# Optimization experiments

Measured on AMD Instinct MI355X. Metric: run time of the kernel, lower is better.

Reference implementation:

```python
import jax, jax.numpy as jnp
import numpy as np
from jax import lax

WINDOW = 40          # plan.window_size
E = 8                # len(plan.expand_feature)
F = 64               # len(plan.feature)
OUT_CH = 128
KERNEL = 5
ALPHA = 0.01         # leaky_relu_alpha
N_LABEL = 1


def time_conv(x, conv_size):
    """x: [N, T, F] -> [N, WINDOW, 5*E] sliding-window stats over first E features."""
    N, T, _ = x.shape
    begin = T - (conv_size + WINDOW - 1)
    xe = x[:, :, :E]                                             # [N, T, E]
    idx = begin + jnp.arange(WINDOW)[:, None] + jnp.arange(conv_size)[None, :]  # [W, C]
    win = xe[:, idx, :]                                          # [N, W, C, E]
    _mean = win.mean(axis=2)                                     # [N, W, E]
    _std = jnp.std(win, axis=2, ddof=1)                          # torch.std is unbiased
    _max = win.max(axis=2)
    _min = win.min(axis=2)
    # rank of last timestep of each window, cross-sectionally over stocks (dim 0)
    last = xe[:, begin + conv_size - 1: begin + conv_size - 1 + WINDOW, :]  # [N, W, E]
    order = jnp.argsort(-last, axis=0)
    rank = jnp.argsort(order, axis=0).astype(x.dtype) / N        # [N, W, E]
    return jnp.concatenate([_mean, _std, rank, _max, _min], axis=2)  # [N, W, 5E]


def setup_inputs() -> dict:
    key = jax.random.key(0)
    k1, k2, k3, k4, k5 = jax.random.split(key, 5)
    N, T = 8000, 64
    in_ch = F + 10 * E  # 144
    x = jax.random.normal(k1, (N, T, F), dtype=jnp.float32)
    conv_w = jax.random.normal(k2, (OUT_CH, in_ch, KERNEL), dtype=jnp.float32) * 0.05
    conv_b = jax.random.normal(k3, (OUT_CH,), dtype=jnp.float32) * 0.05
    lin_in = WINDOW + 1 - KERNEL  # 36
    lin_w = jax.random.normal(k4, (N_LABEL, lin_in), dtype=jnp.float32) * 0.1
    lin_b = jax.random.normal(k5, (N_LABEL,), dtype=jnp.float32) * 0.1
    return {"x": x, "conv_w": conv_w, "conv_b": conv_b, "lin_w": lin_w, "lin_b": lin_b}


def reference(x, conv_w, conv_b, lin_w, lin_b):
    week_x = time_conv(x, conv_size=5)     # [N, W, 5E]
    month_x = time_conv(x, conv_size=20)   # [N, W, 5E]
    xc = jnp.concatenate([x[:, -WINDOW:, :], week_x, month_x], axis=2)  # [N, W, F+10E]
    cnn_x = jnp.transpose(xc, (0, 2, 1))   # [N, C, W]
    part = lax.conv_general_dilated(cnn_x, conv_w, window_strides=(1,),
                                    padding='VALID',
                                    dimension_numbers=('NCH', 'OIH', 'NCH'))
    part = part + conv_b[None, :, None]    # [N, OUT_CH, W+1-K]
    h = part[:, -1, :]                     # last output channel, [N, W+1-K]
    h = jnp.where(h >= 0, h, ALPHA * h)    # leaky relu
    return h @ lin_w.T + lin_b             # [N, N_LABEL]
```

## Files before the change

### kernel.cpp

```cpp
#include <hip/hip_runtime.h>
#include <math.h>

#define NS    8000
#define TT    64
#define FF    64
#define EE    8
#define WIN   40
#define TR    59
#define NBINS 2048

#define XET_SZ  (8*59*8000)
#define RNK_SZ  (8*40*8000)

__global__ __launch_bounds__(256) void k_transpose(const float* __restrict__ x,
                                                   float* __restrict__ xeT) {
    int n = blockIdx.x * 256 + threadIdx.x;
    int r = blockIdx.y;
    if (n >= NS) return;
    const float* row = x + (size_t)n * (TT * FF) + (5 + r) * FF;
    float4 a = *(const float4*)(row);
    float4 b = *(const float4*)(row + 4);
    xeT[(0 * TR + r) * NS + n] = a.x;
    xeT[(1 * TR + r) * NS + n] = a.y;
    xeT[(2 * TR + r) * NS + n] = a.z;
    xeT[(3 * TR + r) * NS + n] = a.w;
    xeT[(4 * TR + r) * NS + n] = b.x;
    xeT[(5 * TR + r) * NS + n] = b.y;
    xeT[(6 * TR + r) * NS + n] = b.z;
    xeT[(7 * TR + r) * NS + n] = b.w;
}

__device__ __forceinline__ int binOf(float v) {
    int b = (int)((v + 4.0f) * 256.0f);
    b = b < 0 ? 0 : b;
    return b > (NBINS - 1) ? (NBINS - 1) : b;
}

__global__ __launch_bounds__(1024) void k_rank(const float* __restrict__ xeT,
                                               float* __restrict__ rankT) {
    const int w = blockIdx.x;
    const int e = blockIdx.y;
    __shared__ unsigned hist[NBINS];
    __shared__ unsigned basev[NBINS];
    __shared__ unsigned bendv[NBINS];
    __shared__ float          sk[NS];
    __shared__ unsigned short si[NS];
    __shared__ unsigned wsum[16];

    const int tid  = threadIdx.x;
    const int lane = tid & 63;
    const int wid  = tid >> 6;
    const float* col = xeT + ((size_t)e * TR + (19 + w)) * NS;

    float val[8];
#pragma unroll
    for (int i = 0; i < 8; i++) {
        int idx = tid + i * 1024;
        val[i] = (idx < NS) ? col[idx] : 0.0f;
    }
    hist[tid] = 0;
    hist[tid + 1024] = 0;
    __syncthreads();

#pragma unroll
    for (int i = 0; i < 8; i++) {
        int idx = tid + i * 1024;
        if (idx < NS) atomicAdd(&hist[binOf(val[i])], 1u);
    }
    __syncthreads();

    unsigned h0 = hist[2 * tid + 0];
    unsigned h1 = hist[2 * tid + 1];
    unsigned cs = h0 + h1;
    unsigned sc = cs;
#pragma unroll
    for (int d = 1; d < 64; d <<= 1) {
        unsigned t2 = __shfl_up(sc, d);
        if (lane >= d) sc += t2;
    }
    if (lane == 63) wsum[wid] = sc;
    __syncthreads();
    unsigned woff = 0;
    for (int i = 0; i < wid; i++) woff += wsum[i];
    unsigned before = woff + (sc - cs);
    {
        int b = 2 * tid;
        bendv[b] = NS - before; before += h0; basev[b] = NS - before;
        hist[b] = basev[b];  b++;
        bendv[b] = NS - before; before += h1; basev[b] = NS - before;
        hist[b] = basev[b];
    }
    __syncthreads();

#pragma unroll
    for (int i = 0; i < 8; i++) {
        int idx = tid + i * 1024;
        if (idx < NS) {
            int b = binOf(val[i]);
            unsigned p = atomicAdd(&hist[b], 1u);
            sk[p] = val[i];
            si[p] = (unsigned short)idx;
        }
    }
    __syncthreads();

    float* outp = rankT + ((size_t)e * WIN + w) * NS;
#pragma unroll 1
    for (int i = 0; i < 8; i++) {
        int p = tid + i * 1024;
        if (p < NS) {
            float v = sk[p];
            unsigned idm = si[p];
            int b = binOf(v);
            unsigned lo = basev[b], hi = bendv[b];
            unsigned c = 0;
            for (unsigned q = lo; q < hi; q++) {
                float u2 = sk[q];
                c += (u2 > v) || (u2 == v && si[q] < idm);
            }
            outp[idm] = (float)(basev[b] + c) / 8000.0f;
        }
    }
}

__global__ __launch_bounds__(256) void k_raw(const float* __restrict__ x,
                                             const float* __restrict__ cw,
                                             float* __restrict__ uraw) {
    const int n    = blockIdx.x * 4 + (threadIdx.x >> 6);
    const int lane = threadIdx.x & 63;
    const int g    = lane >> 4;
    const int l    = lane & 15;
    const float* W = cw + 127 * 144 * 5;

    float wreg[20];
    {
        const float4* Wq = (const float4*)(W + l * 20);
#pragma unroll
        for (int q = 0; q < 5; q++) {
            float4 t = Wq[q];
            wreg[q * 4 + 0] = t.x; wreg[q * 4 + 1] = t.y;
            wreg[q * 4 + 2] = t.z; wreg[q * 4 + 3] = t.w;
        }
    }

    const float* xbase = x + (size_t)n * (TT * FF) + 24 * FF + l * 4;
    float* ubase = uraw + (size_t)n * (WIN * 5);

#pragma unroll 1
    for (int w0 = 0; w0 < WIN; w0 += 4) {
        const int w = w0 + g;
        float4 xv = *(const float4*)(xbase + w * FF);
        float acc[5];
#pragma unroll
        for (int k = 0; k < 5; k++) {
            acc[k] = xv.x * wreg[0 * 5 + k] + xv.y * wreg[1 * 5 + k]
                   + xv.z * wreg[2 * 5 + k] + xv.w * wreg[3 * 5 + k];
        }
#pragma unroll
        for (int d = 1; d < 16; d <<= 1) {
#pragma unroll
            for (int k = 0; k < 5; k++) acc[k] += __shfl_xor(acc[k], d, 64);
        }
        if (l < 5) {
            float v = acc[0];
            if (l == 1) v = acc[1];
            else if (l == 2) v = acc[2];
            else if (l == 3) v = acc[3];
            else if (l == 4) v = acc[4];
            ubase[w * 5 + l] = v;
        }
    }
}

__global__ __launch_bounds__(256) void k_der_final(const float* __restrict__ cw,
                                                   const float* __restrict__ xeT,
                                                   const float* __restrict__ rankT,
                                                   const float* __restrict__ uraw,
                                                   const float* __restrict__ cb,
                                                   const float* __restrict__ lw,
                                                   const float* __restrict__ lb,
                                                   float* __restrict__ outp) {
    __shared__ float red[8][32][37];
    const int tid = threadIdx.x;
    const int e   = tid >> 5;
    const int nl  = tid & 31;
    const int n0  = blockIdx.x * 32;
    const int n   = n0 + nl;
    const float* W = cw + 127 * 144 * 5;

    float gder[36];
#pragma unroll
    for (int j = 0; j < 36; j++) gder[j] = 0.0f;

    const float* col = xeT + (size_t)e * TR * NS + n;
    const float* rkp = rankT + (size_t)e * WIN * NS + n;

    float ring[20];
#pragma unroll
    for (int r = 0; r < 19; r++) ring[r] = col[(size_t)r * NS];

#pragma unroll
    for (int w = 0; w < WIN; w++) {
        ring[(w + 19) % 20] = col[(size_t)(w + 19) * NS];
        float s20 = 0.f, mn20 = ring[0], mx20 = ring[0];
#pragma unroll
        for (int i = 0; i < 20; i++) {
            float v = ring[i];
            s20 += v; mn20 = fminf(mn20, v); mx20 = fmaxf(mx20, v);
        }
        float m20 = s20 * (1.0f / 20.0f);
        float d20 = 0.f;
#pragma unroll
        for (int i = 0; i < 20; i++) { float t = ring[i] - m20; d20 += t * t; }
        float sd20 = sqrtf(d20 * (1.0f / 19.0f));

        float s5 = 0.f, mn5 = ring[(w + 15) % 20], mx5 = mn5;
#pragma unroll
        for (int i = 15; i < 20; i++) {
            float v = ring[(w + i) % 20];
            s5 += v; mn5 = fminf(mn5, v); mx5 = fmaxf(mx5, v);
        }
        float m5 = s5 * 0.2f;
        float d5 = 0.f;
#pragma unroll
        for (int i = 15; i < 20; i++) {
            float t = ring[(w + i) % 20] - m5; d5 += t * t;
        }
        float sd5 = sqrtf(d5 * 0.25f);

        float rk = rkp[(size_t)w * NS];

#pragma unroll
        for (int k = 0; k < 5; k++) {
            int j = w - k;
            if (j >= 0 && j < 36) {
                float uk;
                uk  = m5   * W[(64  + e) * 5 + k];
                uk += sd5  * W[(72  + e) * 5 + k];
                uk += rk   * (W[(80 + e) * 5 + k] + W[(120 + e) * 5 + k]);
                uk += mx5  * W[(88  + e) * 5 + k];
                uk += mn5  * W[(96  + e) * 5 + k];
                uk += m20  * W[(104 + e) * 5 + k];
                uk += sd20 * W[(112 + e) * 5 + k];
                uk += mx20 * W[(128 + e) * 5 + k];
                uk += mn20 * W[(136 + e) * 5 + k];
                gder[j] += uk;
            }
        }
    }

#pragma unroll
    for (int j = 0; j < 36; j++) red[e][nl][j] = gder[j];
    __syncthreads();

    for (int p = tid; p < 32 * 36; p += 256) {
        int nl2 = p / 36, j = p - nl2 * 36;
        float sum = 0.f;
#pragma unroll
        for (int e2 = 0; e2 < 8; e2++) sum += red[e2][nl2][j];
        red[0][nl2][j] = sum;
    }
    __syncthreads();

    if (tid < 32) {
        const float* ur = uraw + (size_t)n * (WIN * 5);
        float b127 = cb[127];
        float acc = lb[0];
#pragma unroll
        for (int j = 0; j < 36; j++) {
            float g = b127 + red[0][tid][j];
#pragma unroll
            for (int k = 0; k < 5; k++) g += ur[(j + k) * 5 + k];
            g = (g >= 0.0f) ? g : 0.01f * g;
            acc += g * lw[j];
        }
        outp[n] = acc;
    }
}

extern "C" void kernel_launch(void* const* d_in, const int* in_sizes, int n_in,
                              void* d_out, int out_size, void* d_ws, size_t ws_size,
                              hipStream_t stream) {
    const float* x  = (const float*)d_in[0];
    const float* cw = (const float*)d_in[1];
    const float* cb = (const float*)d_in[2];
    const float* lw = (const float*)d_in[3];
    const float* lb = (const float*)d_in[4];
    float* outp = (float*)d_out;

    float* ws    = (float*)d_ws;
    float* xeT   = ws;
    float* rankT = ws + XET_SZ;
    float* uraw  = ws + XET_SZ + RNK_SZ;

    k_transpose<<<dim3(32, 59), 256, 0, stream>>>(x, xeT);
    k_rank<<<dim3(WIN, EE), 1024, 0, stream>>>(xeT, rankT);
    k_raw<<<2000, 256, 0, stream>>>(x, cw, uraw);
    k_der_final<<<250, 256, 0, stream>>>(cw, xeT, rankT, uraw, cb, lw, lb, outp);
}
```

Measured before the change: 253.0 us.

## Fuse raw conv projection into transpose, pack rank keys, widen histogram bins

Merges the raw-feature projection of the last conv channel into the transpose kernel, so the separate k_raw launch goes away and x rows already loaded are reused. The rank kernel now uses 8192 finer histogram bins and packs value and index into one 64-bit sortable key, so the tie-break inside a bucket becomes a single integer compare and the bucket ends come from neighbouring bases. The per-channel conv weights are hoisted into registers in the final kernel. Risks are the extra register pressure and uncoalesced per-thread row loads in the fused kernel, plus the larger shared-memory footprint of the 64-bit keys and bigger histogram.

Measured after the change: 244.7 us. 1.03x faster.

```diff
diff --git a/kernel.cpp b/kernel.cpp
--- a/kernel.cpp
+++ b/kernel.cpp
@@ -7,13 +7,15 @@
 #define EE    8
 #define WIN   40
 #define TR    59
-#define NBINS 2048
+#define NBINS 8192
 
 #define XET_SZ  (8*59*8000)
 #define RNK_SZ  (8*40*8000)
 
-__global__ __launch_bounds__(256) void k_transpose(const float* __restrict__ x,
-                                                   float* __restrict__ xeT) {
+__global__ __launch_bounds__(256) void k0(const float* __restrict__ x,
+                                          const float* __restrict__ cw,
+                                          float* __restrict__ xeT,
+                                          float* __restrict__ uraw) {
     int n = blockIdx.x * 256 + threadIdx.x;
     int r = blockIdx.y;
     if (n >= NS) return;
@@ -28,12 +30,40 @@
     xeT[(5 * TR + r) * NS + n] = b.y;
     xeT[(6 * TR + r) * NS + n] = b.z;
     xeT[(7 * TR + r) * NS + n] = b.w;
+
+    if (r >= 19) {
+        const int w = r - 19;
+        const float* W = cw + 127 * 144 * 5;
+        float4 v[16];
+        v[0] = a; v[1] = b;
+#pragma unroll
+        for (int q = 2; q < 16; q++) v[q] = *(const float4*)(row + 4 * q);
+        float acc0 = 0.f, acc1 = 0.f, acc2 = 0.f, acc3 = 0.f, acc4 = 0.f;
+#pragma unroll
+        for (int q = 0; q < 16; q++) {
+            const float* Wq = W + (4 * q) * 5;
+            acc0 += v[q].x * Wq[0]  + v[q].y * Wq[5]  + v[q].z * Wq[10] + v[q].w * Wq[15];
+            acc1 += v[q].x * Wq[1]  + v[q].y * Wq[6]  + v[q].z * Wq[11] + v[q].w * Wq[16];
+            acc2 += v[q].x * Wq[2]  + v[q].y * Wq[7]  + v[q].z * Wq[12] + v[q].w * Wq[17];
+            acc3 += v[q].x * Wq[3]  + v[q].y * Wq[8]  + v[q].z * Wq[13] + v[q].w * Wq[18];
+            acc4 += v[q].x * Wq[4]  + v[q].y * Wq[9]  + v[q].z * Wq[14] + v[q].w * Wq[19];
+        }
+        float* o = uraw + ((size_t)n * WIN + w) * 5;
+        o[0] = acc0; o[1] = acc1; o[2] = acc2; o[3] = acc3; o[4] = acc4;
+    }
 }
 
 __device__ __forceinline__ int binOf(float v) {
-    int b = (int)((v + 4.0f) * 256.0f);
+    int b = (int)((v + 4.0f) * 1024.0f);
     b = b < 0 ? 0 : b;
     return b > (NBINS - 1) ? (NBINS - 1) : b;
+}
+
+__device__ __forceinline__ unsigned long long keyOf(float v, unsigned idx) {
+    unsigned s = __float_as_uint(v);
+    unsigned m = (s & 0x80000000u) ? (~s) : (s | 0x80000000u);
+    unsigned md = ~m;
+    return ((unsigned long long)md << 13) | idx;
 }
 
 __global__ __launch_bounds__(1024) void k_rank(const float* __restrict__ xeT,
@@ -42,9 +72,7 @@
     const int e = blockIdx.y;
     __shared__ unsigned hist[NBINS];
     __shared__ unsigned basev[NBINS];
-    __shared__ unsigned bendv[NBINS];
-    __shared__ float          sk[NS];
-    __shared__ unsigned short si[NS];
+    __shared__ unsigned long long sk[NS];
     __shared__ unsigned wsum[16];
 
     const int tid  = threadIdx.x;
@@ -58,8 +86,8 @@
         int idx = tid + i * 1024;
         val[i] = (idx < NS) ? col[idx] : 0.0f;
     }
-    hist[tid] = 0;
-    hist[tid + 1024] = 0;
+#pragma unroll
+    for (int j = 0; j < 8; j++) hist[tid + j * 1024] = 0;
     __syncthreads();
 
 #pragma unroll
@@ -69,9 +97,12 @@
     }
     __syncthreads();
 
-    unsigned h0 = hist[2 * tid + 0];
-    unsigned h1 = hist[2 * tid + 1];
-    unsigned cs = h0 + h1;
+    unsigned h[8];
+#pragma unroll
+    for (int j = 0; j < 8; j++) h[j] = hist[8 * tid + j];
+    unsigned cs = 0;
+#pragma unroll
+    for (int j = 0; j < 8; j++) cs += h[j];
     unsigned sc = cs;
 #pragma unroll
     for (int d = 1; d < 64; d <<= 1) {
@@ -82,13 +113,14 @@
     __syncthreads();
     unsigned woff = 0;
     for (int i = 0; i < wid; i++) woff += wsum[i];
-    unsigned before = woff + (sc - cs);
-    {
-        int b = 2 * tid;
-        bendv[b] = NS - before; before += h0; basev[b] = NS - before;
-        hist[b] = basev[b];  b++;
-        bendv[b] = NS - before; before += h1; basev[b] = NS - before;
-        hist[b] = basev[b];
+    unsigned bsum = woff + (sc - cs);
+#pragma unroll
+    for (int j = 0; j < 8; j++) {
+        int b = 8 * tid + j;
+        unsigned bv = NS - bsum - h[j];
+        basev[b] = bv;
+        hist[b]  = bv;
+        bsum += h[j];
     }
     __syncthreads();
 
@@ -98,8 +130,7 @@
         if (idx < NS) {
             int b = binOf(val[i]);
             unsigned p = atomicAdd(&hist[b], 1u);
-            sk[p] = val[i];
-            si[p] = (unsigned short)idx;
+            sk[p] = keyOf(val[i], (unsigned)idx);
         }
     }
     __syncthreads();
@@ -109,65 +140,17 @@
     for (int i = 0; i < 8; i++) {
         int p = tid + i * 1024;
         if (p < NS) {
-            float v = sk[p];
-            unsigned idm = si[p];
+            unsigned long long k64 = sk[p];
+            unsigned md = (unsigned)(k64 >> 13);
+            unsigned m  = ~md;
+            unsigned s  = (m & 0x80000000u) ? (m ^ 0x80000000u) : (~m);
+            float v = __uint_as_float(s);
             int b = binOf(v);
-            unsigned lo = basev[b], hi = bendv[b];
+            unsigned lo = basev[b];
+            unsigned hi = (b == 0) ? NS : basev[b - 1];
             unsigned c = 0;
-            for (unsigned q = lo; q < hi; q++) {
-                float u2 = sk[q];
-                c += (u2 > v) || (u2 == v && si[q] < idm);
-            }
-            outp[idm] = (float)(basev[b] + c) / 8000.0f;
-        }
-    }
-}
-
-__global__ __launch_bounds__(256) void k_raw(const float* __restrict__ x,
-                                             const float* __restrict__ cw,
-                                             float* __restrict__ uraw) {
-    const int n    = blockIdx.x * 4 + (threadIdx.x >> 6);
-    const int lane = threadIdx.x & 63;
-    const int g    = lane >> 4;
-    const int l    = lane & 15;
-    const float* W = cw + 127 * 144 * 5;
-
-    float wreg[20];
-    {
-        const float4* Wq = (const float4*)(W + l * 20);
-#pragma unroll
-        for (int q = 0; q < 5; q++) {
-            float4 t = Wq[q];
-            wreg[q * 4 + 0] = t.x; wreg[q * 4 + 1] = t.y;
-            wreg[q * 4 + 2] = t.z; wreg[q * 4 + 3] = t.w;
-        }
-    }
-
-    const float* xbase = x + (size_t)n * (TT * FF) + 24 * FF + l * 4;
-    float* ubase = uraw + (size_t)n * (WIN * 5);
-
-#pragma unroll 1
-    for (int w0 = 0; w0 < WIN; w0 += 4) {
-        const int w = w0 + g;
-        float4 xv = *(const float4*)(xbase + w * FF);
-        float acc[5];
-#pragma unroll
-        for (int k = 0; k < 5; k++) {
-            acc[k] = xv.x * wreg[0 * 5 + k] + xv.y * wreg[1 * 5 + k]
-                   + xv.z * wreg[2 * 5 + k] + xv.w * wreg[3 * 5 + k];
-        }
-#pragma unroll
-        for (int d = 1; d < 16; d <<= 1) {
-#pragma unroll
-            for (int k = 0; k < 5; k++) acc[k] += __shfl_xor(acc[k], d, 64);
-        }
-        if (l < 5) {
-            float v = acc[0];
-            if (l == 1) v = acc[1];
-            else if (l == 2) v = acc[2];
-            else if (l == 3) v = acc[3];
-            else if (l == 4) v = acc[4];
-            ubase[w * 5 + l] = v;
+            for (unsigned q = lo; q < hi; q++) c += (sk[q] < k64);
+            outp[k64 & 8191u] = (float)(basev[b] + c) * (1.0f / 8000.0f);
         }
     }
 }
@@ -188,6 +171,20 @@
     const int n   = n0 + nl;
     const float* W = cw + 127 * 144 * 5;
 
+    float wm5[5], wsd5[5], wrk[5], wmx5[5], wmn5[5], wm20[5], wsd20[5], wmx20[5], wmn20[5];
+#pragma unroll
+    for (int k = 0; k < 5; k++) {
+        wm5[k]   = W[(64  + e) * 5 + k];
+        wsd5[k]  = W[(72  + e) * 5 + k];
+        wrk[k]   = W[(80  + e) * 5 + k] + W[(120 + e) * 5 + k];
+        wmx5[k]  = W[(88  + e) * 5 + k];
+        wmn5[k]  = W[(96  + e) * 5 + k];
+        wm20[k]  = W[(104 + e) * 5 + k];
+        wsd20[k] = W[(112 + e) * 5 + k];
+        wmx20[k] = W[(128 + e) * 5 + k];
+        wmn20[k] = W[(136 + e) * 5 + k];
+    }
+
     float gder[36];
 #pragma unroll
     for (int j = 0; j < 36; j++) gder[j] = 0.0f;
@@ -235,15 +232,15 @@
             int j = w - k;
             if (j >= 0 && j < 36) {
                 float uk;
-                uk  = m5   * W[(64  + e) * 5 + k];
-                uk += sd5  * W[(72  + e) * 5 + k];
-                uk += rk   * (W[(80 + e) * 5 + k] + W[(120 + e) * 5 + k]);
-                uk += mx5  * W[(88  + e) * 5 + k];
-                uk += mn5  * W[(96  + e) * 5 + k];
-                uk += m20  * W[(104 + e) * 5 + k];
-                uk += sd20 * W[(112 + e) * 5 + k];
-                uk += mx20 * W[(128 + e) * 5 + k];
-                uk += mn20 * W[(136 + e) * 5 + k];
+                uk  = m5   * wm5[k];
+                uk += sd5  * wsd5[k];
+                uk += rk   * wrk[k];
+                uk += mx5  * wmx5[k];
+                uk += mn5  * wmn5[k];
+                uk += m20  * wm20[k];
+                uk += sd20 * wsd20[k];
+                uk += mx20 * wmx20[k];
+                uk += mn20 * wmn20[k];
                 gder[j] += uk;
             }
         }
@@ -293,8 +290,7 @@
     float* rankT = ws + XET_SZ;
     float* uraw  = ws + XET_SZ + RNK_SZ;
 
-    k_transpose<<<dim3(32, 59), 256, 0, stream>>>(x, xeT);
+    k0<<<dim3(32, 59), 256, 0, stream>>>(x, cw, xeT, uraw);
     k_rank<<<dim3(WIN, EE), 1024, 0, stream>>>(xeT, rankT);
-    k_raw<<<2000, 256, 0, stream>>>(x, cw, uraw);
     k_der_final<<<250, 256, 0, stream>>>(cw, xeT, rankT, uraw, cb, lw, lb, outp);
 }
```
